# Kernel tuning notes

Measured on AMD Instinct MI355X. Metric: run time of the kernel, lower is better.

Reference implementation:

```python
import jax, jax.numpy as jnp
import numpy as np

DIM = 2048
STATE = 2048
SEL_H = 1024
B = 16384


def setup_inputs() -> dict:
    key = jax.random.key(0)
    ks = jax.random.split(key, 7)
    def lin(k, out_f, in_f):
        return jax.random.normal(k, (out_f, in_f), dtype=jnp.float32) / np.sqrt(in_f)
    return {
        "x_t": jax.random.normal(ks[0], (B, DIM), dtype=jnp.float32),
        "h_prev": jax.random.normal(ks[1], (B, STATE), dtype=jnp.float32),
        "W_in": lin(ks[2], STATE, DIM),
        "W_sel_in": lin(ks[3], SEL_H, DIM),
        "W_sel_out": lin(ks[4], 4 * STATE, SEL_H),
        "W_out": lin(ks[5], DIM, STATE),
        "d": jnp.ones((STATE,), dtype=jnp.float32),
    }


def reference(x_t, h_prev, W_in, W_sel_in, W_sel_out, W_out, d):
    # u_t = in_proj(x_t): [B, state]
    u_t = x_t @ W_in.T
    # selector: silu(x @ W_sel_in.T) @ W_sel_out.T -> [B, 4*state]
    sel_h = jax.nn.silu(x_t @ W_sel_in.T)
    sel = sel_h @ W_sel_out.T
    a_raw, b_raw, c_raw, d_raw = jnp.split(sel, 4, axis=-1)
    a_t = jax.nn.sigmoid(a_raw)
    b_t = jnp.tanh(b_raw)
    c_t = jnp.tanh(c_raw)
    d_t = jax.nn.sigmoid(d_raw)
    h_t = a_t * h_prev + b_t * u_t
    y_t = c_t * h_t + d[None, :] * d_t * u_t
    out = y_t @ W_out.T  # [B, dim]
    return (out, h_t)
```

## Files before the change

kernel.cpp:

```cpp
#include <hip/hip_runtime.h>
#include <hip/hip_bf16.h>
#include <cstdint>

#define NB    16384
#define DIMX  2048
#define STATE 2048
#define SELH  1024

typedef unsigned short u16;
typedef short  short8_t __attribute__((ext_vector_type(8)));
typedef float  f32x4    __attribute__((ext_vector_type(4)));

__device__ __forceinline__ u16 f2bf(float f) {
  unsigned u = __builtin_bit_cast(unsigned, f);
  u += 0x7fffu + ((u >> 16) & 1u);
  return (u16)(u >> 16);
}
__device__ __forceinline__ float bf2f(u16 h) {
  unsigned u = ((unsigned)h) << 16;
  return __builtin_bit_cast(float, u);
}
__device__ __forceinline__ float sigmoidf_(float x) { return 1.f / (1.f + __expf(-x)); }
__device__ __forceinline__ float tanhf_(float x)    { return 2.f / (1.f + __expf(-2.f * x)) - 1.f; }

__device__ __forceinline__ f32x4 mfma_bf16(short8_t a, short8_t b, f32x4 c) {
  return __builtin_amdgcn_mfma_f32_16x16x32_bf16(a, b, c, 0, 0, 0);
}

__device__ __forceinline__ void gload16(const void* g, const void* l) {
  __builtin_amdgcn_global_load_lds(
      (const __attribute__((address_space(1))) unsigned int*)(uintptr_t)g,
      (__attribute__((address_space(3))) unsigned int*)(unsigned int)(uintptr_t)l,
      16, 0, 0);
}

__global__ __launch_bounds__(256) void k_f32_to_bf16(const float* __restrict__ src,
                                                     u16* __restrict__ dst, int n4) {
  int i = blockIdx.x * blockDim.x + threadIdx.x;
  int stride = gridDim.x * blockDim.x;
  for (; i < n4; i += stride) {
    float4 v = ((const float4*)src)[i];
    ushort4 o;
    o.x = f2bf(v.x); o.y = f2bf(v.y); o.z = f2bf(v.z); o.w = f2bf(v.w);
    ((ushort4*)dst)[i] = o;
  }
}

template <int EPI, int KD, int NCOLS>
__global__ __launch_bounds__(512, 2) void k_gemm256(const u16* __restrict__ A,
                                                    const u16* __restrict__ Bsrc,
                                                    float* __restrict__ f32out,
                                                    u16* __restrict__ bfout,
                                                    const float* __restrict__ hprev,
                                                    const u16* __restrict__ ubf,
                                                    const float* __restrict__ dvec) {
  __shared__ __align__(16) char smem[131072];
  const int tid = threadIdx.x;
  const int w = tid >> 6, l = tid & 63;
  const int wr = w >> 2, wc = w & 3;
  const int bx = blockIdx.x, by = blockIdx.y;
  const int m0 = by * 256;

  const unsigned aAddr0 = (unsigned)(wr * 16384 + (l & 15) * 128 +
                                     (((l >> 4) * 16) ^ ((l & 7) << 4)));
  const unsigned aAddr1 = aAddr0 ^ 64u;
  const unsigned bAddr0 = (unsigned)(65536 + (wc * 64 + (l & 15)) * 64 +
                                     (((l >> 4) * 16) ^ ((l & 3) << 4)));
  const unsigned bAddr1 = bAddr0 + 16384u;

  const int rA = tid >> 3;
  const int kA = ((tid & 7) ^ ((tid >> 3) & 7)) * 8;
  const u16* aSrc = A + (size_t)(m0 + rA) * KD + kA;

  const int rB = tid >> 2;
  const int kB = ((tid & 3) ^ ((tid >> 2) & 3)) * 8;
  size_t bRow0, bRow1;
  if constexpr (EPI <= 2) {
    bRow0 = (size_t)bx * 256 + rB;
    bRow1 = bRow0 + 128;
  } else {
    const int q0 = (EPI == 3) ? 0 : 2;
    const int s0 = bx * 128;
    const int sub0 = rB & 63, wcb0 = rB >> 6;
    const int r1 = rB + 128;
    const int sub1 = r1 & 63, wcb1 = r1 >> 6;
    bRow0 = (size_t)(q0 + (sub0 >> 5)) * STATE + s0 + wcb0 * 32 + (sub0 & 31);
    bRow1 = (size_t)(q0 + (sub1 >> 5)) * STATE + s0 + wcb1 * 32 + (sub1 & 31);
  }
  const u16* bSrc0 = Bsrc + bRow0 * KD + kB;
  const u16* bSrc1 = Bsrc + bRow1 * KD + kB;

  auto stageA = [&](int k0n, int rh, unsigned dstD) {
    const u16* sp = aSrc + (size_t)rh * 128 * KD + k0n;
    gload16(sp,               smem + dstD + (unsigned)rh * 16384u + (unsigned)tid * 16u);
    gload16(sp + 64 * KD,     smem + dstD + (unsigned)rh * 16384u + 8192u + (unsigned)tid * 16u);
  };
  auto stageB = [&](int k0n, int kh, unsigned dstD) {
    const int kk = k0n + kh * 32;
    gload16(bSrc0 + kk, smem + 65536u + dstD + (unsigned)kh * 16384u + (unsigned)tid * 16u);
    gload16(bSrc1 + kk, smem + 65536u + dstD + (unsigned)kh * 16384u + 8192u + (unsigned)tid * 16u);
  };

  f32x4 acc[8][4];
#pragma unroll
  for (int i = 0; i < 8; ++i)
#pragma unroll
    for (int j = 0; j < 4; ++j) acc[i][j] = f32x4{0.f, 0.f, 0.f, 0.f};

  short8_t av[8], bvN[2], bvM[2];

#define LOAD_AV(D, KK)                                                         \
  _Pragma("unroll") for (int mf = 0; mf < 8; ++mf)                             \
      av[mf] = *(const short8_t*)(smem + ((KK) ? aAddr1 : aAddr0) +            \
                                  (D) * 32768u + mf * 2048u);
#define LOAD_BV(R, I, NF, D, KK)                                               \
  R[I] = *(const short8_t*)(smem + ((KK) ? bAddr1 : bAddr0) + (D) * 32768u +   \
                            (NF) * 1024u);
#define MFMA8x2(BV, NFA, NFB)                                                  \
  __builtin_amdgcn_s_setprio(1);                                               \
  _Pragma("unroll") for (int mf = 0; mf < 8; ++mf) {                           \
    acc[mf][NFA] = mfma_bf16(av[mf], BV[0], acc[mf][NFA]);                     \
    acc[mf][NFB] = mfma_bf16(av[mf], BV[1], acc[mf][NFB]);                     \
  }                                                                            \
  __builtin_amdgcn_s_setprio(0);

#define KTILE(D, K0, DO_STAGE, K0N, LASTT)                                     \
  {                                                                            \
                                                           \
    LOAD_AV(D, 0);                                                             \
    LOAD_BV(bvN, 0, 0, D, 0); LOAD_BV(bvN, 1, 1, D, 0);                        \
    if (DO_STAGE) stageA(K0N, 0, (D ^ 1) * 32768u);                            \
    __builtin_amdgcn_s_barrier();                                              \
    MFMA8x2(bvN, 0, 1);                                                        \
    __builtin_amdgcn_s_barrier();                                              \
                                                           \
    LOAD_BV(bvM, 0, 2, D, 0); LOAD_BV(bvM, 1, 3, D, 0);                        \
    if (DO_STAGE) stageA(K0N, 1, (D ^ 1) * 32768u);                            \
    if (LASTT) { asm volatile("s_waitcnt vmcnt(0)" ::: "memory"); }            \
    else       { asm volatile("s_waitcnt vmcnt(4)" ::: "memory"); }            \
    __builtin_amdgcn_s_barrier();                                              \
    MFMA8x2(bvM, 2, 3);                                                        \
    __builtin_amdgcn_s_barrier();                                              \
                                                           \
    LOAD_AV(D, 1);                                                             \
    LOAD_BV(bvM, 0, 2, D, 1); LOAD_BV(bvM, 1, 3, D, 1);                        \
    if (DO_STAGE) stageB(K0N, 0, (D ^ 1) * 32768u);                            \
    __builtin_amdgcn_s_barrier();                                              \
    MFMA8x2(bvM, 2, 3);                                                        \
    __builtin_amdgcn_s_barrier();                                              \
                                                           \
    LOAD_BV(bvN, 0, 0, D, 1); LOAD_BV(bvN, 1, 1, D, 1);                        \
    if (DO_STAGE) stageB(K0N, 1, (D ^ 1) * 32768u);                            \
    if (!LASTT) { asm volatile("s_waitcnt vmcnt(2)" ::: "memory"); }           \
    __builtin_amdgcn_s_barrier();                                              \
    MFMA8x2(bvN, 0, 1);                                                        \
    __builtin_amdgcn_s_barrier();                                              \
  }

  stageA(0, 0, 0u); stageA(0, 1, 0u); stageB(0, 0, 0u); stageB(0, 1, 0u);
  asm volatile("s_waitcnt vmcnt(2)" ::: "memory");
  __builtin_amdgcn_s_barrier();

  constexpr int NT = KD / 64;
  int k0 = 0;
#pragma unroll 1
  for (int T = 0; T < NT - 2; T += 2) {
    KTILE(0, k0, true, k0 + 64, false);
    KTILE(1, k0 + 64, true, k0 + 128, false);
    k0 += 128;
  }
  KTILE(0, k0, true, k0 + 64, false);
  KTILE(1, k0 + 64, false, 0, true);

#undef KTILE
#undef MFMA8x2
#undef LOAD_BV
#undef LOAD_AV

  const int rbase = m0 + wr * 128 + ((l >> 4) << 2);
  if constexpr (EPI <= 2) {
    const int cbase = bx * 256 + wc * 64 + (l & 15);
#pragma unroll
    for (int mf = 0; mf < 8; ++mf)
#pragma unroll
      for (int nf = 0; nf < 4; ++nf)
#pragma unroll
        for (int r = 0; r < 4; ++r) {
          const int row = rbase + mf * 16 + r;
          const int col = cbase + nf * 16;
          const size_t idx = (size_t)row * NCOLS + col;
          const float v = acc[mf][nf][r];
          if constexpr (EPI == 0) {
            bfout[idx] = f2bf(v);
          } else if constexpr (EPI == 1) {
            bfout[idx] = f2bf(v * sigmoidf_(v));
          } else {
            f32out[idx] = v;
          }
        }
  } else {
    const int sbase = bx * 128 + wc * 32 + (l & 15);
#pragma unroll
    for (int mf = 0; mf < 8; ++mf)
#pragma unroll
      for (int nf = 0; nf < 2; ++nf)
#pragma unroll
        for (int r = 0; r < 4; ++r) {
          const int row = rbase + mf * 16 + r;
          const int s = sbase + nf * 16;
          const size_t idx = (size_t)row * STATE + s;
          const float own = acc[mf][nf][r];
          const float oth = acc[mf][nf + 2][r];
          const float uu = bf2f(ubf[idx]);
          if constexpr (EPI == 3) {
            f32out[idx] = sigmoidf_(own) * hprev[idx] + tanhf_(oth) * uu;
          } else {
            bfout[idx] = f2bf(tanhf_(own) * hprev[idx] +
                              dvec[s] * sigmoidf_(oth) * uu);
          }
        }
  }
}

extern "C" void kernel_launch(void* const* d_in, const int* in_sizes, int n_in,
                              void* d_out, int out_size, void* d_ws, size_t ws_size,
                              hipStream_t stream) {
  const float* x   = (const float*)d_in[0];
  const float* h0  = (const float*)d_in[1];
  const float* Win = (const float*)d_in[2];
  const float* Wsi = (const float*)d_in[3];
  const float* Wso = (const float*)d_in[4];
  const float* Wou = (const float*)d_in[5];
  const float* dv  = (const float*)d_in[6];
  float* out  = (float*)d_out;
  float* hout = out + (size_t)NB * DIMX;

  u16* ws = (u16*)d_ws;
  size_t o = 0;
  u16* xb   = ws + o; o += (size_t)NB * DIMX;
  u16* ub   = ws + o; o += (size_t)NB * STATE;
  u16* yb   = ws + o; o += (size_t)NB * STATE;
  u16* sh   = ws + o; o += (size_t)NB * SELH;
  u16* wib  = ws + o; o += (size_t)STATE * DIMX;
  u16* wsib = ws + o; o += (size_t)SELH * DIMX;
  u16* wsob = ws + o; o += (size_t)4 * STATE * SELH;
  u16* wob  = ws + o; o += (size_t)DIMX * STATE;

  k_f32_to_bf16<<<1024, 256, 0, stream>>>(x,   xb,   NB * DIMX / 4);
  k_f32_to_bf16<<<256,  256, 0, stream>>>(Win, wib,  STATE * DIMX / 4);
  k_f32_to_bf16<<<128,  256, 0, stream>>>(Wsi, wsib, SELH * DIMX / 4);
  k_f32_to_bf16<<<512,  256, 0, stream>>>(Wso, wsob, 4 * STATE * SELH / 4);
  k_f32_to_bf16<<<256,  256, 0, stream>>>(Wou, wob,  DIMX * STATE / 4);

  const dim3 blk(512);
  k_gemm256<0, DIMX, STATE><<<dim3(STATE / 256, NB / 256), blk, 0, stream>>>(
      xb, wib, nullptr, ub, nullptr, nullptr, nullptr);
  k_gemm256<1, DIMX, SELH><<<dim3(SELH / 256, NB / 256), blk, 0, stream>>>(
      xb, wsib, nullptr, sh, nullptr, nullptr, nullptr);
  k_gemm256<3, SELH, 0><<<dim3(STATE / 128, NB / 256), blk, 0, stream>>>(
      sh, wsob, hout, nullptr, h0, ub, nullptr);
  k_gemm256<4, SELH, 0><<<dim3(STATE / 128, NB / 256), blk, 0, stream>>>(
      sh, wsob, nullptr, yb, hout, ub, dv);
  k_gemm256<2, STATE, DIMX><<<dim3(DIMX / 256, NB / 256), blk, 0, stream>>>(
      yb, wob, out, nullptr, nullptr, nullptr, nullptr);
}
```

Before: 811.0 us.

## Fuse the two selector-output GEMMs into one with all four gates per tile

The selector-output GEMM was split into two launches: one produced a/b and wrote h_t, and the other produced c/d and re-read h_t to compute y. Now a single launch gathers the a, b, c and d weight rows for 64 state columns into each 256-wide tile. Its epilogue computes h_t and y_t together, which removes the second pass over ub and h. Loads of d are hoisted per thread and LDS reads get alignment hints. The grid doubles in columns so total MFMA work is unchanged, and extra traffic on hprev, ub and hout is avoided.

```diff
diff --git a/kernel.cpp b/kernel.cpp
--- a/kernel.cpp
+++ b/kernel.cpp
@@ -33,6 +33,8 @@
       (__attribute__((address_space(3))) unsigned int*)(unsigned int)(uintptr_t)l,
       16, 0, 0);
 }
+
+#define LDS_V(p) (*(const short8_t*)__builtin_assume_aligned((const void*)(p), 16))
 
 __global__ __launch_bounds__(256) void k_f32_to_bf16(const float* __restrict__ src,
                                                      u16* __restrict__ dst, int n4) {
@@ -79,21 +81,18 @@
     bRow0 = (size_t)bx * 256 + rB;
     bRow1 = bRow0 + 128;
   } else {
-    const int q0 = (EPI == 3) ? 0 : 2;
-    const int s0 = bx * 128;
-    const int sub0 = rB & 63, wcb0 = rB >> 6;
+    const int s0 = bx * 64;
     const int r1 = rB + 128;
-    const int sub1 = r1 & 63, wcb1 = r1 >> 6;
-    bRow0 = (size_t)(q0 + (sub0 >> 5)) * STATE + s0 + wcb0 * 32 + (sub0 & 31);
-    bRow1 = (size_t)(q0 + (sub1 >> 5)) * STATE + s0 + wcb1 * 32 + (sub1 & 31);
+    bRow0 = (size_t)((rB >> 4) & 3) * STATE + s0 + (rB >> 6) * 16 + (rB & 15);
+    bRow1 = (size_t)((r1 >> 4) & 3) * STATE + s0 + (r1 >> 6) * 16 + (r1 & 15);
   }
   const u16* bSrc0 = Bsrc + bRow0 * KD + kB;
   const u16* bSrc1 = Bsrc + bRow1 * KD + kB;
 
   auto stageA = [&](int k0n, int rh, unsigned dstD) {
     const u16* sp = aSrc + (size_t)rh * 128 * KD + k0n;
-    gload16(sp,               smem + dstD + (unsigned)rh * 16384u + (unsigned)tid * 16u);
-    gload16(sp + 64 * KD,     smem + dstD + (unsigned)rh * 16384u + 8192u + (unsigned)tid * 16u);
+    gload16(sp,           smem + dstD + (unsigned)rh * 16384u + (unsigned)tid * 16u);
+    gload16(sp + 64 * KD, smem + dstD + (unsigned)rh * 16384u + 8192u + (unsigned)tid * 16u);
   };
   auto stageB = [&](int k0n, int kh, unsigned dstD) {
     const int kk = k0n + kh * 32;
@@ -111,11 +110,9 @@
 
 #define LOAD_AV(D, KK)                                                         \
   _Pragma("unroll") for (int mf = 0; mf < 8; ++mf)                             \
-      av[mf] = *(const short8_t*)(smem + ((KK) ? aAddr1 : aAddr0) +            \
-                                  (D) * 32768u + mf * 2048u);
+      av[mf] = LDS_V(smem + ((KK) ? aAddr1 : aAddr0) + (D) * 32768u + mf * 2048u);
 #define LOAD_BV(R, I, NF, D, KK)                                               \
-  R[I] = *(const short8_t*)(smem + ((KK) ? bAddr1 : bAddr0) + (D) * 32768u +   \
-                            (NF) * 1024u);
+  R[I] = LDS_V(smem + ((KK) ? bAddr1 : bAddr0) + (D) * 32768u + (NF) * 1024u);
 #define MFMA8x2(BV, NFA, NFB)                                                  \
   __builtin_amdgcn_s_setprio(1);                                               \
   _Pragma("unroll") for (int mf = 0; mf < 8; ++mf) {                           \
@@ -199,26 +196,24 @@
           }
         }
   } else {
-    const int sbase = bx * 128 + wc * 32 + (l & 15);
+    const int s = bx * 64 + wc * 16 + (l & 15);
+    const float dval = dvec[s];
 #pragma unroll
     for (int mf = 0; mf < 8; ++mf)
 #pragma unroll
-      for (int nf = 0; nf < 2; ++nf)
-#pragma unroll
-        for (int r = 0; r < 4; ++r) {
-          const int row = rbase + mf * 16 + r;
-          const int s = sbase + nf * 16;
-          const size_t idx = (size_t)row * STATE + s;
-          const float own = acc[mf][nf][r];
-          const float oth = acc[mf][nf + 2][r];
-          const float uu = bf2f(ubf[idx]);
-          if constexpr (EPI == 3) {
-            f32out[idx] = sigmoidf_(own) * hprev[idx] + tanhf_(oth) * uu;
-          } else {
-            bfout[idx] = f2bf(tanhf_(own) * hprev[idx] +
-                              dvec[s] * sigmoidf_(oth) * uu);
-          }
-        }
+      for (int r = 0; r < 4; ++r) {
+        const int row = rbase + mf * 16 + r;
+        const size_t idx = (size_t)row * STATE + s;
+        const float a  = acc[mf][0][r];
+        const float b  = acc[mf][1][r];
+        const float c  = acc[mf][2][r];
+        const float dd = acc[mf][3][r];
+        const float uu = bf2f(ubf[idx]);
+        const float hp = hprev[idx];
+        const float h = sigmoidf_(a) * hp + tanhf_(b) * uu;
+        f32out[idx] = h;
+        bfout[idx] = f2bf(tanhf_(c) * h + dval * sigmoidf_(dd) * uu);
+      }
   }
 }
 
@@ -257,10 +252,8 @@
       xb, wib, nullptr, ub, nullptr, nullptr, nullptr);
   k_gemm256<1, DIMX, SELH><<<dim3(SELH / 256, NB / 256), blk, 0, stream>>>(
       xb, wsib, nullptr, sh, nullptr, nullptr, nullptr);
-  k_gemm256<3, SELH, 0><<<dim3(STATE / 128, NB / 256), blk, 0, stream>>>(
-      sh, wsob, hout, nullptr, h0, ub, nullptr);
-  k_gemm256<4, SELH, 0><<<dim3(STATE / 128, NB / 256), blk, 0, stream>>>(
-      sh, wsob, nullptr, yb, hout, ub, dv);
+  k_gemm256<3, SELH, 0><<<dim3(STATE / 64, NB / 256), blk, 0, stream>>>(
+      sh, wsob, hout, yb, h0, ub, dv);
   k_gemm256<2, STATE, DIMX><<<dim3(DIMX / 256, NB / 256), blk, 0, stream>>>(
       yb, wob, out, nullptr, nullptr, nullptr, nullptr);
 }
```

Result: no change. 798.2 us (-1.6%).
